# Kernel optimization log

Hardware: AMD Instinct MI355X
Metric: run time of the kernel (lower is better)

## Reference

```python
import jax, jax.numpy as jnp
import numpy as np
from jax import lax

# Conv3d(in_dim, in_dim, kernel=(1,3,3), padding=(0,1,1)) == per-time-slice 3x3 conv mixing channels

def _conv3d(x, w, b):
    # x: [B, C, T, W, H], w: [O, I, 1, 3, 3], b: [O]
    y = lax.conv_general_dilated(
        x, w,
        window_strides=(1, 1, 1),
        padding=[(0, 0), (1, 1), (1, 1)],
        dimension_numbers=("NCDHW", "OIDHW", "NCDHW"),
    )
    return y + b[None, :, None, None, None]


def setup_inputs() -> dict:
    key = jax.random.key(0)
    ks = jax.random.split(key, 8)
    B, C, T, W, H = 8, 64, 16, 64, 64
    fan = C * 1 * 3 * 3
    bound = 1.0 / np.sqrt(fan)  # torch Conv3d default init range
    x = jax.random.normal(ks[0], (B, C, T, W, H), dtype=jnp.float32)
    wq = jax.random.uniform(ks[1], (C, C, 1, 3, 3), jnp.float32, -bound, bound)
    wk = jax.random.uniform(ks[2], (C, C, 1, 3, 3), jnp.float32, -bound, bound)
    wv = jax.random.uniform(ks[3], (C, C, 1, 3, 3), jnp.float32, -bound, bound)
    bq = jax.random.uniform(ks[4], (C,), jnp.float32, -bound, bound)
    bk = jax.random.uniform(ks[5], (C,), jnp.float32, -bound, bound)
    bv = jax.random.uniform(ks[6], (C,), jnp.float32, -bound, bound)
    # torch init is gamma=0 (identity output); use nonzero so reference exercises the full path
    gamma = jax.random.normal(ks[7], (1,), dtype=jnp.float32) * 0.1
    return {"x": x, "wq": wq, "wk": wk, "wv": wv,
            "bq": bq, "bk": bk, "bv": bv, "gamma": gamma}


def reference(x, wq, wk, wv, bq, bk, bv, gamma):
    B, C, T, W, H = x.shape
    WH = W * H
    q = _conv3d(x, wq, bq).reshape(B, C, T, WH)
    k = _conv3d(x, wk, bk).reshape(B, C, T, WH)
    v = _conv3d(x, wv, bv).reshape(B, C, T, WH)
    # Original: (q[...,:,None] @ k[...,None,:]) @ v[...,:,None]  -> rank-1 energy, no softmax.
    # Exact reassociation: out_i = q_i * sum_j(k_j * v_j), avoiding the [WH, WH] matrix.
    s = jnp.sum(k * v, axis=-1, keepdims=True)  # [B, C, T, 1]
    out = (q * s).reshape(B, C, T, W, H)
    return gamma[0] * out + x
```

## Files before the change

kernel.cpp:

```cpp
#include <hip/hip_runtime.h>
#include <hip/hip_bf16.h>
#include <stdint.h>

typedef __attribute__((ext_vector_type(8))) short bf16x8;
typedef __attribute__((ext_vector_type(4))) float f32x4v;
typedef __attribute__((ext_vector_type(16))) float f32x16;

#define CH_STRIDE 65536

__device__ __forceinline__ uint16_t f2bf(float f) {
  uint32_t u = __builtin_bit_cast(uint32_t, f);
  u = (u + 0x7FFFu + ((u >> 16) & 1u)) >> 16;
  return (uint16_t)u;
}
__device__ __forceinline__ float bf2f(uint32_t b) {
  return __builtin_bit_cast(float, b << 16);
}
__device__ __forceinline__ uint16_t cvt_bf(float f) {
  return __builtin_bit_cast(uint16_t, __float2bfloat16(f));
}

#define MFMA32(a, b, c) __builtin_amdgcn_mfma_f32_32x32x16_bf16(a, b, c, 0, 0, 0)
#define LGKM0 asm volatile("s_waitcnt lgkmcnt(0)" ::: "memory")
#define BAR __builtin_amdgcn_s_barrier()
#define SCHED0 __builtin_amdgcn_sched_barrier(0)

#define LDSX_BYTES (6 * 8 * 66 * 16)

__device__ __forceinline__ uint32_t swz(uint32_t b) {
  return b ^ (((b >> 7) & 7u) << 4);
}

__device__ __forceinline__ bf16x8 ldx(const uint8_t* ldsx, int r6, int oct, int ci) {
  return *(const bf16x8*)(ldsx + swz((uint32_t)((r6 * 8 + oct) * 66 + ci) * 16u));
}

__device__ __forceinline__ void stage_x(uint8_t* ldsx, const float* xs, int w0, int tid) {
  if (tid < 96) {
    int r6 = tid >> 4, rem = tid & 15;
    int oct = rem >> 1, side = rem & 1;
    bf16x8 z = {};
    *(bf16x8*)(ldsx + swz((uint32_t)((r6 * 8 + oct) * 66 + side * 65) * 16u)) = z;
  }
  #pragma unroll
  for (int k = 0; k < 3; ++k) {
    int u = tid + k * 256;
    int r6 = u >> 7, oct = (u >> 4) & 7, g = u & 15;
    int w = w0 - 1 + r6;
    uint32_t base = (uint32_t)((r6 * 8 + oct) * 66 + 4 * g + 1) * 16u;
    if ((unsigned)w < 64u) {
      const float* p = xs + (size_t)(oct * 8) * CH_STRIDE + w * 64 + 4 * g;
      f32x4v v[8];
      #pragma unroll
      for (int j = 0; j < 8; ++j) v[j] = *(const f32x4v*)(p + (size_t)j * CH_STRIDE);
      #pragma unroll
      for (int c = 0; c < 4; ++c) {
        bf16x8 frag;
        #pragma unroll
        for (int q = 0; q < 4; ++q) {
          frag[2 * q]     = (short)cvt_bf(v[2 * q][c]);
          frag[2 * q + 1] = (short)cvt_bf(v[2 * q + 1][c]);
        }
        *(bf16x8*)(ldsx + swz(base + (uint32_t)c * 16u)) = frag;
      }
    } else {
      bf16x8 z = {};
      #pragma unroll
      for (int c = 0; c < 4; ++c)
        *(bf16x8*)(ldsx + swz(base + (uint32_t)c * 16u)) = z;
    }
  }
}

__device__ __forceinline__ bf16x8 ldw_kv(const uint8_t* ldsw, int oct, int rowloc) {
  return *(const bf16x8*)(ldsw + (uint32_t)(oct * 128 + rowloc) * 16u);
}
__device__ __forceinline__ void ldw_g_kv(bf16x8* r, const uint16_t* wkv, int tap, int tid) {
  #pragma unroll
  for (int k = 0; k < 4; ++k)
    r[k] = *(const bf16x8*)(wkv + ((size_t)tap * 1024 + tid + k * 256) * 8);
}
__device__ __forceinline__ void stw_kv(uint8_t* ldsw, const bf16x8* r, int tid) {
  #pragma unroll
  for (int k = 0; k < 4; ++k)
    *(bf16x8*)(ldsw + (uint32_t)(tid + k * 256) * 16u) = r[k];
}

__device__ __forceinline__ bf16x8 ldw_q(const uint8_t* ldsw, int oct, int row) {
  return *(const bf16x8*)(ldsw + (uint32_t)(oct * 64 + row) * 16u);
}
__device__ __forceinline__ void ldw_g_q(bf16x8* r, const uint16_t* wq, int tap, int tid) {
  #pragma unroll
  for (int k = 0; k < 2; ++k)
    r[k] = *(const bf16x8*)(wq + ((size_t)tap * 512 + tid + k * 256) * 8);
}
__device__ __forceinline__ void stw_q(uint8_t* ldsw, const bf16x8* r, int tid) {
  #pragma unroll
  for (int k = 0; k < 2; ++k)
    *(bf16x8*)(ldsw + (uint32_t)(tid + k * 256) * 16u) = r[k];
}

__global__ void prep_weights(const float* __restrict__ wq, const float* __restrict__ wk,
                             const float* __restrict__ wv, uint16_t* __restrict__ wout) {
  int i = blockIdx.x * 256 + threadIdx.x;
  if (i >= 110592) return;
  if (i < 36864) {
    int tap = i >> 12, oct = (i >> 9) & 7, row = (i >> 3) & 63, j = i & 7;
    wout[i] = f2bf(wq[(row * 64 + oct * 8 + j) * 9 + tap]);
  } else {
    int m = i - 36864;
    int tap = m >> 13, oct = (m >> 10) & 7, rl = (m >> 3) & 127, j = m & 7;
    const float* src = (rl < 64) ? wk : wv;
    wout[i] = f2bf(src[((rl & 63) * 64 + oct * 8 + j) * 9 + tap]);
  }
}

__global__ __launch_bounds__(256, 2) void kv_s_kernel(
    const float* __restrict__ x, const uint16_t* __restrict__ wkv,
    const float* __restrict__ bk, const float* __restrict__ bv,
    float* __restrict__ s_out) {
  extern __shared__ uint8_t lds[];
  uint8_t* ldsx = lds;
  uint8_t* ldsw = lds + LDSX_BYTES;
  const int tid = threadIdx.x;
  const int l = tid & 63, ng = tid >> 6;
  int bid = (int)(blockIdx.x & 7) * 256 + (int)(blockIdx.x >> 3);
  const int rg = bid & 15, slice = bid >> 4;
  const int b = slice >> 4, t = slice & 15;
  const int w0 = rg * 4;
  const float* xs = x + ((size_t)b * 1024 + t) * 4096;
  const int lm = l & 31, lh = l >> 5;

  stage_x(ldsx, xs, w0, tid);
  bf16x8 r[4];
  ldw_g_kv(r, wkv, 0, tid);
  stw_kv(ldsw, r, tid);
  ldw_g_kv(r, wkv, 1, tid);
  SCHED0; LGKM0; BAR; SCHED0;

  f32x16 accK[2][2], accV[2][2];
  #pragma unroll
  for (int mt = 0; mt < 2; ++mt)
    #pragma unroll
    for (int nt = 0; nt < 2; ++nt)
      #pragma unroll
      for (int q = 0; q < 16; ++q) { accK[mt][nt][q] = 0.f; accV[mt][nt][q] = 0.f; }

  #pragma unroll
  for (int tap = 0; tap < 9; ++tap) {
    const int dy = tap / 3, dx = tap % 3;
    __builtin_amdgcn_s_setprio(1);
    #pragma unroll
    for (int s = 0; s < 4; ++s) {
      int oct = s * 2 + lh;
      bf16x8 aK0 = ldw_kv(ldsw, oct, lm);
      bf16x8 aK1 = ldw_kv(ldsw, oct, 32 + lm);
      bf16x8 aV0 = ldw_kv(ldsw, oct, 64 + lm);
      bf16x8 aV1 = ldw_kv(ldsw, oct, 96 + lm);
      bf16x8 b0  = ldx(ldsx, ng + dy, oct, lm + dx);
      bf16x8 b1  = ldx(ldsx, ng + dy, oct, 32 + lm + dx);
      accK[0][0] = MFMA32(aK0, b0, accK[0][0]);
      accK[0][1] = MFMA32(aK0, b1, accK[0][1]);
      accK[1][0] = MFMA32(aK1, b0, accK[1][0]);
      accK[1][1] = MFMA32(aK1, b1, accK[1][1]);
      accV[0][0] = MFMA32(aV0, b0, accV[0][0]);
      accV[0][1] = MFMA32(aV0, b1, accV[0][1]);
      accV[1][0] = MFMA32(aV1, b0, accV[1][0]);
      accV[1][1] = MFMA32(aV1, b1, accV[1][1]);
    }
    __builtin_amdgcn_s_setprio(0);
    if (tap < 8) {
      SCHED0; BAR;
      stw_kv(ldsw, r, tid);
      if (tap < 7) ldw_g_kv(r, wkv, tap + 2, tid);
      SCHED0; LGKM0; BAR; SCHED0;
    }
  }

  __syncthreads();
  float* red = (float*)ldsx;
  #pragma unroll
  for (int q = 0; q < 16; ++q) {
    int cl = (q & 3) + 8 * (q >> 2) + 4 * lh;
    #pragma unroll
    for (int mt = 0; mt < 2; ++mt) {
      int c = mt * 32 + cl;
      float bkc = bk[c], bvc = bv[c];
      float p = (accK[mt][0][q] + bkc) * (accV[mt][0][q] + bvc)
              + (accK[mt][1][q] + bkc) * (accV[mt][1][q] + bvc);
      red[c * 132 + ng * 32 + lm] = p;
    }
  }
  __syncthreads();
  if (tid < 64) {
    const f32x4v* rp = (const f32x4v*)(red + tid * 132);
    f32x4v a4 = {0.f, 0.f, 0.f, 0.f};
    #pragma unroll
    for (int j = 0; j < 32; ++j) a4 += rp[j];
    atomicAdd(s_out + (b * 16 + t) * 64 + tid, a4[0] + a4[1] + a4[2] + a4[3]);
  }
}

__global__ __launch_bounds__(256, 2) void q_out_kernel(
    const float* __restrict__ x, const uint16_t* __restrict__ wq,
    const float* __restrict__ bq, const float* __restrict__ s_in,
    const float* __restrict__ gamma, float* __restrict__ out) {
  extern __shared__ uint8_t lds[];
  uint8_t* ldsx = lds;
  uint8_t* ldsw = lds + LDSX_BYTES;
  const int tid = threadIdx.x;
  const int l = tid & 63, ng = tid >> 6;
  int bid = (int)(blockIdx.x & 7) * 256 + (int)(blockIdx.x >> 3);
  const int rg = bid & 15, slice = bid >> 4;
  const int b = slice >> 4, t = slice & 15;
  const int w0 = rg * 4;
  const float* xs = x + ((size_t)b * 1024 + t) * 4096;
  const int lm = l & 31, lh = l >> 5;

  stage_x(ldsx, xs, w0, tid);
  bf16x8 r[2];
  ldw_g_q(r, wq, 0, tid);
  stw_q(ldsw, r, tid);
  ldw_g_q(r, wq, 1, tid);
  SCHED0; LGKM0; BAR; SCHED0;

  f32x16 acc[2][2];
  #pragma unroll
  for (int mt = 0; mt < 2; ++mt)
    #pragma unroll
    for (int nt = 0; nt < 2; ++nt)
      #pragma unroll
      for (int q = 0; q < 16; ++q) acc[mt][nt][q] = 0.f;

  #pragma unroll
  for (int tap = 0; tap < 9; ++tap) {
    const int dy = tap / 3, dx = tap % 3;
    __builtin_amdgcn_s_setprio(1);
    #pragma unroll
    for (int s = 0; s < 4; ++s) {
      int oct = s * 2 + lh;
      bf16x8 a0 = ldw_q(ldsw, oct, lm);
      bf16x8 a1 = ldw_q(ldsw, oct, 32 + lm);
      bf16x8 b0 = ldx(ldsx, ng + dy, oct, lm + dx);
      bf16x8 b1 = ldx(ldsx, ng + dy, oct, 32 + lm + dx);
      acc[0][0] = MFMA32(a0, b0, acc[0][0]);
      acc[0][1] = MFMA32(a0, b1, acc[0][1]);
      acc[1][0] = MFMA32(a1, b0, acc[1][0]);
      acc[1][1] = MFMA32(a1, b1, acc[1][1]);
    }
    __builtin_amdgcn_s_setprio(0);
    if (tap < 8) {
      SCHED0; BAR;
      stw_q(ldsw, r, tid);
      if (tap < 7) ldw_g_q(r, wq, tap + 2, tid);
      SCHED0; LGKM0; BAR; SCHED0;
    }
  }

  float g = gamma[0];
  const float* sb = s_in + (b * 16 + t) * 64;
  int w = w0 + ng;
  #pragma unroll
  for (int mt = 0; mt < 2; ++mt) {
    #pragma unroll
    for (int q = 0; q < 16; ++q) {
      int cl = (q & 3) + 8 * (q >> 2) + 4 * lh;
      int c  = mt * 32 + cl;
      float qb = bq[c], sc = sb[c];
      #pragma unroll
      for (int nt = 0; nt < 2; ++nt) {
        int h = nt * 32 + lm;
        uint32_t xb = (uint32_t)(((ng + 1) * 8 + (c >> 3)) * 66 + (h + 1)) * 16u
                    + (uint32_t)(c & 7) * 2u;
        float xv = bf2f(*(const uint16_t*)(ldsx + swz(xb)));
        size_t idx = ((size_t)(b * 64 + c) * 16 + t) * 4096 + (size_t)w * 64 + h;
        out[idx] = g * (acc[mt][nt][q] + qb) * sc + xv;
      }
    }
  }
}

extern "C" void kernel_launch(void* const* d_in, const int* in_sizes, int n_in,
                              void* d_out, int out_size, void* d_ws, size_t ws_size,
                              hipStream_t stream) {
  const float* x   = (const float*)d_in[0];
  const float* wq  = (const float*)d_in[1];
  const float* wk  = (const float*)d_in[2];
  const float* wv  = (const float*)d_in[3];
  const float* bq  = (const float*)d_in[4];
  const float* bk  = (const float*)d_in[5];
  const float* bv  = (const float*)d_in[6];
  const float* gam = (const float*)d_in[7];

  uint16_t* wbf = (uint16_t*)d_ws;
  float* sbuf   = (float*)((uint8_t*)d_ws + 221184);

  hipMemsetAsync(sbuf, 0, 8 * 16 * 64 * sizeof(float), stream);
  prep_weights<<<(110592 + 255) / 256, 256, 0, stream>>>(wq, wk, wv, wbf);
  kv_s_kernel<<<2048, 256, LDSX_BYTES + 16384, stream>>>(x, wbf + 36864, bk, bv, sbuf);
  q_out_kernel<<<2048, 256, LDSX_BYTES + 8192, stream>>>(x, wbf, bq, sbuf, gam, (float*)d_out);
}
```

Before: 156.0 us.

## Split kv_s_kernel output channels across 8 waves with 512-thread blocks

The K/V conv kernel moves from 4 to 8 waves per block. Each wave now owns one 32-channel half of K and V instead of both halves, which halves per-wave accumulators (64 fewer VGPRs) and spreads x staging and weight loads over twice as many threads. The aim is more concurrent waves and better latency hiding for the MFMA loop. The cost is duplicated B-fragment LDS reads across the two channel-half waves and larger block-wide barriers.

After: 156.5 us. No clear change (+0.3%).

```diff
diff --git a/kernel.cpp b/kernel.cpp
--- a/kernel.cpp
+++ b/kernel.cpp
@@ -35,55 +35,63 @@
   return *(const bf16x8*)(ldsx + swz((uint32_t)((r6 * 8 + oct) * 66 + ci) * 16u));
 }
 
-__device__ __forceinline__ void stage_x(uint8_t* ldsx, const float* xs, int w0, int tid) {
+__device__ __forceinline__ void stage_unit(uint8_t* ldsx, const float* xs, int w0, int u) {
+  int r6 = u >> 7, oct = (u >> 4) & 7, g = u & 15;
+  int w = w0 - 1 + r6;
+  uint32_t base = (uint32_t)((r6 * 8 + oct) * 66 + 4 * g + 1) * 16u;
+  if ((unsigned)w < 64u) {
+    const float* p = xs + (size_t)(oct * 8) * CH_STRIDE + w * 64 + 4 * g;
+    f32x4v v[8];
+    #pragma unroll
+    for (int j = 0; j < 8; ++j) v[j] = *(const f32x4v*)(p + (size_t)j * CH_STRIDE);
+    #pragma unroll
+    for (int c = 0; c < 4; ++c) {
+      bf16x8 frag;
+      #pragma unroll
+      for (int q = 0; q < 4; ++q) {
+        frag[2 * q]     = (short)cvt_bf(v[2 * q][c]);
+        frag[2 * q + 1] = (short)cvt_bf(v[2 * q + 1][c]);
+      }
+      *(bf16x8*)(ldsx + swz(base + (uint32_t)c * 16u)) = frag;
+    }
+  } else {
+    bf16x8 z = {};
+    #pragma unroll
+    for (int c = 0; c < 4; ++c)
+      *(bf16x8*)(ldsx + swz(base + (uint32_t)c * 16u)) = z;
+  }
+}
+__device__ __forceinline__ void stage_halo(uint8_t* ldsx, int tid) {
   if (tid < 96) {
     int r6 = tid >> 4, rem = tid & 15;
     int oct = rem >> 1, side = rem & 1;
     bf16x8 z = {};
     *(bf16x8*)(ldsx + swz((uint32_t)((r6 * 8 + oct) * 66 + side * 65) * 16u)) = z;
   }
-  #pragma unroll
-  for (int k = 0; k < 3; ++k) {
-    int u = tid + k * 256;
-    int r6 = u >> 7, oct = (u >> 4) & 7, g = u & 15;
-    int w = w0 - 1 + r6;
-    uint32_t base = (uint32_t)((r6 * 8 + oct) * 66 + 4 * g + 1) * 16u;
-    if ((unsigned)w < 64u) {
-      const float* p = xs + (size_t)(oct * 8) * CH_STRIDE + w * 64 + 4 * g;
-      f32x4v v[8];
-      #pragma unroll
-      for (int j = 0; j < 8; ++j) v[j] = *(const f32x4v*)(p + (size_t)j * CH_STRIDE);
-      #pragma unroll
-      for (int c = 0; c < 4; ++c) {
-        bf16x8 frag;
-        #pragma unroll
-        for (int q = 0; q < 4; ++q) {
-          frag[2 * q]     = (short)cvt_bf(v[2 * q][c]);
-          frag[2 * q + 1] = (short)cvt_bf(v[2 * q + 1][c]);
-        }
-        *(bf16x8*)(ldsx + swz(base + (uint32_t)c * 16u)) = frag;
-      }
-    } else {
-      bf16x8 z = {};
-      #pragma unroll
-      for (int c = 0; c < 4; ++c)
-        *(bf16x8*)(ldsx + swz(base + (uint32_t)c * 16u)) = z;
-    }
-  }
+}
+__device__ __forceinline__ void stage_x256(uint8_t* ldsx, const float* xs, int w0, int tid) {
+  stage_halo(ldsx, tid);
+  #pragma unroll
+  for (int k = 0; k < 3; ++k) stage_unit(ldsx, xs, w0, tid + k * 256);
+}
+__device__ __forceinline__ void stage_x512(uint8_t* ldsx, const float* xs, int w0, int tid) {
+  stage_halo(ldsx, tid);
+  stage_unit(ldsx, xs, w0, tid);
+  if (tid < 256) stage_unit(ldsx, xs, w0, 512 + tid);
 }
 
 __device__ __forceinline__ bf16x8 ldw_kv(const uint8_t* ldsw, int oct, int rowloc) {
   return *(const bf16x8*)(ldsw + (uint32_t)(oct * 128 + rowloc) * 16u);
 }
-__device__ __forceinline__ void ldw_g_kv(bf16x8* r, const uint16_t* wkv, int tap, int tid) {
-  #pragma unroll
-  for (int k = 0; k < 4; ++k)
-    r[k] = *(const bf16x8*)(wkv + ((size_t)tap * 1024 + tid + k * 256) * 8);
-}
-__device__ __forceinline__ void stw_kv(uint8_t* ldsw, const bf16x8* r, int tid) {
-  #pragma unroll
-  for (int k = 0; k < 4; ++k)
-    *(bf16x8*)(ldsw + (uint32_t)(tid + k * 256) * 16u) = r[k];
+__device__ __forceinline__ void ldw_g_kv2(bf16x8* r, const uint16_t* wkv, int tap, int tid) {
+  #pragma unroll
+  for (int k = 0; k < 2; ++k)
+    r[k] = *(const bf16x8*)(wkv + ((size_t)tap * 1024 + tid + k * 512) * 8);
+}
+__device__ __forceinline__ void stw_kv2(uint8_t* ldsw, const bf16x8* r, int tid) {
+  #pragma unroll
+  for (int k = 0; k < 2; ++k)
+    *(bf16x8*)(ldsw + (uint32_t)(tid + k * 512) * 16u) = r[k];
 }
 
 __device__ __forceinline__ bf16x8 ldw_q(const uint8_t* ldsw, int oct, int row) {
@@ -115,7 +123,7 @@
   }
 }
 
-__global__ __launch_bounds__(256, 2) void kv_s_kernel(
+__global__ __launch_bounds__(512, 4) void kv_s_kernel(
     const float* __restrict__ x, const uint16_t* __restrict__ wkv,
     const float* __restrict__ bk, const float* __restrict__ bv,
     float* __restrict__ s_out) {
@@ -123,7 +131,9 @@
   uint8_t* ldsx = lds;
   uint8_t* ldsw = lds + LDSX_BYTES;
   const int tid = threadIdx.x;
-  const int l = tid & 63, ng = tid >> 6;
+  const int l = tid & 63;
+  const int wid = tid >> 6;
+  const int ng = wid & 3, mg = wid >> 2;
   int bid = (int)(blockIdx.x & 7) * 256 + (int)(blockIdx.x >> 3);
   const int rg = bid & 15, slice = bid >> 4;
   const int b = slice >> 4, t = slice & 15;
@@ -131,20 +141,18 @@
   const float* xs = x + ((size_t)b * 1024 + t) * 4096;
   const int lm = l & 31, lh = l >> 5;
 
-  stage_x(ldsx, xs, w0, tid);
-  bf16x8 r[4];
-  ldw_g_kv(r, wkv, 0, tid);
-  stw_kv(ldsw, r, tid);
-  ldw_g_kv(r, wkv, 1, tid);
+  stage_x512(ldsx, xs, w0, tid);
+  bf16x8 r[2];
+  ldw_g_kv2(r, wkv, 0, tid);
+  stw_kv2(ldsw, r, tid);
+  ldw_g_kv2(r, wkv, 1, tid);
   SCHED0; LGKM0; BAR; SCHED0;
 
-  f32x16 accK[2][2], accV[2][2];
-  #pragma unroll
-  for (int mt = 0; mt < 2; ++mt)
-    #pragma unroll
-    for (int nt = 0; nt < 2; ++nt)
-      #pragma unroll
-      for (int q = 0; q < 16; ++q) { accK[mt][nt][q] = 0.f; accV[mt][nt][q] = 0.f; }
+  f32x16 accK[2], accV[2];
+  #pragma unroll
+  for (int nt = 0; nt < 2; ++nt)
+    #pragma unroll
+    for (int q = 0; q < 16; ++q) { accK[nt][q] = 0.f; accV[nt][q] = 0.f; }
 
   #pragma unroll
   for (int tap = 0; tap < 9; ++tap) {
@@ -153,43 +161,34 @@
     #pragma unroll
     for (int s = 0; s < 4; ++s) {
       int oct = s * 2 + lh;
-      bf16x8 aK0 = ldw_kv(ldsw, oct, lm);
-      bf16x8 aK1 = ldw_kv(ldsw, oct, 32 + lm);
-      bf16x8 aV0 = ldw_kv(ldsw, oct, 64 + lm);
-      bf16x8 aV1 = ldw_kv(ldsw, oct, 96 + lm);
-      bf16x8 b0  = ldx(ldsx, ng + dy, oct, lm + dx);
-      bf16x8 b1  = ldx(ldsx, ng + dy, oct, 32 + lm + dx);
-      accK[0][0] = MFMA32(aK0, b0, accK[0][0]);
-      accK[0][1] = MFMA32(aK0, b1, accK[0][1]);
-      accK[1][0] = MFMA32(aK1, b0, accK[1][0]);
-      accK[1][1] = MFMA32(aK1, b1, accK[1][1]);
-      accV[0][0] = MFMA32(aV0, b0, accV[0][0]);
-      accV[0][1] = MFMA32(aV0, b1, accV[0][1]);
-      accV[1][0] = MFMA32(aV1, b0, accV[1][0]);
-      accV[1][1] = MFMA32(aV1, b1, accV[1][1]);
+      bf16x8 aK = ldw_kv(ldsw, oct, mg * 32 + lm);
+      bf16x8 aV = ldw_kv(ldsw, oct, 64 + mg * 32 + lm);
+      bf16x8 b0 = ldx(ldsx, ng + dy, oct, lm + dx);
+      bf16x8 b1 = ldx(ldsx, ng + dy, oct, 32 + lm + dx);
+      accK[0] = MFMA32(aK, b0, accK[0]);
+      accK[1] = MFMA32(aK, b1, accK[1]);
+      accV[0] = MFMA32(aV, b0, accV[0]);
+      accV[1] = MFMA32(aV, b1, accV[1]);
     }
     __builtin_amdgcn_s_setprio(0);
     if (tap < 8) {
       SCHED0; BAR;
-      stw_kv(ldsw, r, tid);
-      if (tap < 7) ldw_g_kv(r, wkv, tap + 2, tid);
+      stw_kv2(ldsw, r, tid);
+      if (tap < 7) ldw_g_kv2(r, wkv, tap + 2, tid);
       SCHED0; LGKM0; BAR; SCHED0;
     }
   }
 
   __syncthreads();
-  float* red = (float*)ldsx;
+  float* red = (float*)lds;
   #pragma unroll
   for (int q = 0; q < 16; ++q) {
     int cl = (q & 3) + 8 * (q >> 2) + 4 * lh;
-    #pragma unroll
-    for (int mt = 0; mt < 2; ++mt) {
-      int c = mt * 32 + cl;
-      float bkc = bk[c], bvc = bv[c];
-      float p = (accK[mt][0][q] + bkc) * (accV[mt][0][q] + bvc)
-              + (accK[mt][1][q] + bkc) * (accV[mt][1][q] + bvc);
-      red[c * 132 + ng * 32 + lm] = p;
-    }
+    int c = mg * 32 + cl;
+    float bkc = bk[c], bvc = bv[c];
+    float p = (accK[0][q] + bkc) * (accV[0][q] + bvc)
+            + (accK[1][q] + bkc) * (accV[1][q] + bvc);
+    red[c * 132 + ng * 32 + lm] = p;
   }
   __syncthreads();
   if (tid < 64) {
@@ -217,7 +216,7 @@
   const float* xs = x + ((size_t)b * 1024 + t) * 4096;
   const int lm = l & 31, lh = l >> 5;
 
-  stage_x(ldsx, xs, w0, tid);
+  stage_x256(ldsx, xs, w0, tid);
   bf16x8 r[2];
   ldw_g_q(r, wq, 0, tid);
   stw_q(ldsw, r, tid);
@@ -297,6 +296,6 @@
 
   hipMemsetAsync(sbuf, 0, 8 * 16 * 64 * sizeof(float), stream);
   prep_weights<<<(110592 + 255) / 256, 256, 0, stream>>>(wq, wk, wv, wbf);
-  kv_s_kernel<<<2048, 256, LDSX_BYTES + 16384, stream>>>(x, wbf + 36864, bk, bv, sbuf);
+  kv_s_kernel<<<2048, 512, LDSX_BYTES + 16384, stream>>>(x, wbf + 36864, bk, bv, sbuf);
   q_out_kernel<<<2048, 256, LDSX_BYTES + 8192, stream>>>(x, wbf, bq, sbuf, gam, (float*)d_out);
 }
```
